# Kernel optimization log

Measured on AMD Instinct MI355X. Metric: run time of the kernel, lower is better.

## Reference

```python
import jax, jax.numpy as jnp
import numpy as np

MIN_RANGE, MAX_RANGE = -128.0, 127.0
B, S, F_IN, F_OUT = 4, 2048, 4096, 4096
ROUNDS, FACTOR = 12, 2  # 4096 = 2**12 -> 12 prime factors of 2
NBLK = F_IN // FACTOR   # 2048 blocks of 2x2 per round


def setup_inputs() -> dict:
    key = jax.random.key(0)
    ks = jax.random.split(key, 5)
    x = jax.random.normal(ks[0], (B, S, F_IN), jnp.float32)
    weight = jax.random.normal(ks[1], (F_OUT, F_IN), jnp.float32) * (1.0 / np.sqrt(F_IN))
    bias = jax.random.normal(ks[2], (F_OUT,), jnp.float32)
    perm_keys = jax.random.split(ks[3], ROUNDS)
    permutations = jnp.stack([jax.random.permutation(k, F_IN) for k in perm_keys])  # (ROUNDS, F_IN) int32
    # random 2x2 orthogonal blocks via batched QR (stand-in for ortho_group.rvs)
    a = jax.random.normal(ks[4], (ROUNDS, NBLK, FACTOR, FACTOR), jnp.float32)
    matrices, _ = jnp.linalg.qr(a)  # (ROUNDS, NBLK, FACTOR, FACTOR)
    return {"x": x, "weight": weight, "bias": bias,
            "matrices": matrices, "permutations": permutations}


def _rotate(v, permutations, matrices):
    # v: (..., F_IN). Each round: permute features, then block-diagonal orthogonal matmul.
    for r in range(ROUNDS):
        v = v[..., permutations[r]]
        lead = v.shape[:-1]
        vb = v.reshape(lead + (NBLK, FACTOR))
        vb = jnp.einsum('kij,...kj->...ki', matrices[r], vb)
        v = vb.reshape(lead + (F_IN,))
    return v


def _quant_dequant(t):
    # per-tensor asymmetric quantization to [MIN_RANGE, MAX_RANGE] then dequant
    lo = t.min()
    hi = t.max()
    scale = (hi - lo) / (MAX_RANGE - MIN_RANGE)
    q = jnp.clip(jnp.round((t - lo) / scale) + MIN_RANGE, MIN_RANGE, MAX_RANGE)
    return (q - MIN_RANGE) * scale + lo


def reference(x, weight, bias, matrices, permutations):
    # permuted_x = permute_op(x.mT).mT  <=>  rotate along the feature (last) dim
    x_rot = _rotate(x, permutations, matrices)          # (B, S, F_IN)
    # permuted_weight = permute_op(W.mT, inv_mT).mT; for orthogonal blocks inv.mT == M
    w_rot = _rotate(weight, permutations, matrices)     # (F_OUT, F_IN)
    xq = _quant_dequant(x_rot)
    wq = _quant_dequant(w_rot)
    return jnp.einsum('bsf,of->bso', xq, wq) + bias     # (B, S, F_OUT)
```

## Files before the change

kernel.cpp:

```cpp
#include <hip/hip_runtime.h>

#define F_DIM  4096
#define NROUNDS 12
#define GM     8192
#define GN     4096
#define GK     4096
#define BK     64
#define NIT    (GK / BK)

typedef short short8 __attribute__((ext_vector_type(8)));
typedef float f32x4  __attribute__((ext_vector_type(4)));
typedef unsigned short us8 __attribute__((ext_vector_type(8)));
typedef unsigned short ushortT;

typedef __attribute__((address_space(3))) void lds_void;
typedef const __attribute__((address_space(1))) void glob_void;

__device__ __forceinline__ unsigned ordf(float f) {
    unsigned u = __float_as_uint(f);
    return (u & 0x80000000u) ? ~u : (u | 0x80000000u);
}
__device__ __forceinline__ float unordf(unsigned u) {
    unsigned v = (u & 0x80000000u) ? (u & 0x7fffffffu) : ~u;
    return __uint_as_float(v);
}
__device__ __forceinline__ unsigned f2bf(float f) {
    unsigned u = __float_as_uint(f);
    return ((u + 0x7fffu + ((u >> 16) & 1u)) >> 16) & 0xffffu;
}

__global__ void init_mm_kernel(unsigned* mm) {
    if (threadIdx.x < 4) mm[threadIdx.x] = (threadIdx.x & 1) ? 0u : 0xFFFFFFFFu;
}

__global__ __launch_bounds__(256)
void rotate_store_kernel(const float* __restrict__ src,
                         const int*   __restrict__ perms,
                         const float* __restrict__ mats,
                         unsigned*    __restrict__ mm,
                         ushortT*     __restrict__ dst_hi,
                         ushortT*     __restrict__ dst_lo)
{
    __shared__ float4 buf[F_DIM];
    const int t = threadIdx.x;
    const size_t r0 = (size_t)blockIdx.x * 4;
    const int2*   pbase = (const int2*)perms;
    const float4* mbase = (const float4*)mats;

    const float2* s0 = (const float2*)(src + (r0 + 0) * F_DIM);
    const float2* s1 = (const float2*)(src + (r0 + 1) * F_DIM);
    const float2* s2 = (const float2*)(src + (r0 + 2) * F_DIM);
    const float2* s3 = (const float2*)(src + (r0 + 3) * F_DIM);
    #pragma unroll
    for (int q = 0; q < 8; ++q) {
        const int e = t + q * 256;
        float2 a = s0[e], b = s1[e], c = s2[e], d = s3[e];
        buf[e]        = make_float4(a.x, b.x, c.x, d.x);
        buf[e + 2048] = make_float4(a.y, b.y, c.y, d.y);
    }
    __syncthreads();

    int2 pA[8], pB[8];
    float4 mA[8], mB[8];
    #pragma unroll
    for (int q = 0; q < 8; ++q) { int k = t + q * 256; pA[q] = pbase[k]; mA[q] = mbase[k]; }

    #pragma unroll 1
    for (int r = 0; r < NROUNDS; r += 2) {
        float4 va[8], vb[8];
        #pragma unroll
        for (int q = 0; q < 8; ++q) {
            int fa = pA[q].x, fb = pA[q].y;
            va[q] = buf[(fa >> 1) + ((fa & 1) << 11)];
            vb[q] = buf[(fb >> 1) + ((fb & 1) << 11)];
        }
        {
            const int2*   pr = pbase + (size_t)(r + 1) * 2048;
            const float4* mr = mbase + (size_t)(r + 1) * 2048;
            #pragma unroll
            for (int q = 0; q < 8; ++q) { int k = t + q * 256; pB[q] = pr[k]; mB[q] = mr[k]; }
        }
        __syncthreads();
        #pragma unroll
        for (int q = 0; q < 8; ++q) {
            const int k = t + q * 256;
            float4 A = va[q], B = vb[q], M = mA[q];
            buf[k]        = make_float4(M.x*A.x + M.y*B.x, M.x*A.y + M.y*B.y,
                                        M.x*A.z + M.y*B.z, M.x*A.w + M.y*B.w);
            buf[k + 2048] = make_float4(M.z*A.x + M.w*B.x, M.z*A.y + M.w*B.y,
                                        M.z*A.z + M.w*B.z, M.z*A.w + M.w*B.w);
        }
        __syncthreads();

        #pragma unroll
        for (int q = 0; q < 8; ++q) {
            int fa = pB[q].x, fb = pB[q].y;
            va[q] = buf[(fa >> 1) + ((fa & 1) << 11)];
            vb[q] = buf[(fb >> 1) + ((fb & 1) << 11)];
        }
        if (r + 2 < NROUNDS) {
            const int2*   pr = pbase + (size_t)(r + 2) * 2048;
            const float4* mr = mbase + (size_t)(r + 2) * 2048;
            #pragma unroll
            for (int q = 0; q < 8; ++q) { int k = t + q * 256; pA[q] = pr[k]; mA[q] = mr[k]; }
        }
        __syncthreads();
        #pragma unroll
        for (int q = 0; q < 8; ++q) {
            const int k = t + q * 256;
            float4 A = va[q], B = vb[q], M = mB[q];
            buf[k]        = make_float4(M.x*A.x + M.y*B.x, M.x*A.y + M.y*B.y,
                                        M.x*A.z + M.y*B.z, M.x*A.w + M.y*B.w);
            buf[k + 2048] = make_float4(M.z*A.x + M.w*B.x, M.z*A.y + M.w*B.y,
                                        M.z*A.z + M.w*B.z, M.z*A.w + M.w*B.w);
        }
        __syncthreads();
    }

    float lmin = __FLT_MAX__, lmax = -__FLT_MAX__;
    #pragma unroll
    for (int q = 0; q < 8; ++q) {
        const int e = t + q * 256;
        float4 f0 = buf[e];
        float4 f1 = buf[e + 2048];
        lmin = fminf(lmin, fminf(fminf(f0.x, f0.y), fminf(f0.z, f0.w)));
        lmin = fminf(lmin, fminf(fminf(f1.x, f1.y), fminf(f1.z, f1.w)));
        lmax = fmaxf(lmax, fmaxf(fmaxf(f0.x, f0.y), fmaxf(f0.z, f0.w)));
        lmax = fmaxf(lmax, fmaxf(fmaxf(f1.x, f1.y), fmaxf(f1.z, f1.w)));
        const float vr[4][2] = {{f0.x, f1.x}, {f0.y, f1.y}, {f0.z, f1.z}, {f0.w, f1.w}};
        #pragma unroll
        for (int i = 0; i < 4; ++i) {
            unsigned u0 = __float_as_uint(vr[i][0]);
            unsigned u1 = __float_as_uint(vr[i][1]);
            ((unsigned*)(dst_hi + (r0 + i) * F_DIM))[e] = (u0 >> 16) | (u1 & 0xffff0000u);
            ((unsigned*)(dst_lo + (r0 + i) * F_DIM))[e] = (u0 & 0xffffu) | (u1 << 16);
        }
    }
    #pragma unroll
    for (int off = 32; off > 0; off >>= 1) {
        lmin = fminf(lmin, __shfl_down(lmin, off));
        lmax = fmaxf(lmax, __shfl_down(lmax, off));
    }
    if ((t & 63) == 0) {
        atomicMin(&mm[0], ordf(lmin));
        atomicMax(&mm[1], ordf(lmax));
    }
}

__global__ __launch_bounds__(256)
void quant_kernel(ushortT* __restrict__ hi, const ushortT* __restrict__ lo,
                  const unsigned* __restrict__ mm, unsigned nx_chunks)
{
    const unsigned i = blockIdx.x * 256 + threadIdx.x;
    const int sel = (i < nx_chunks) ? 0 : 2;
    const float lov = unordf(mm[sel]);
    const float hiv = unordf(mm[sel + 1]);
    const float scale = (hiv - lov) / 255.0f;
    us8 h = *(const us8*)(hi + (size_t)i * 8);
    us8 l = *(const us8*)(lo + (size_t)i * 8);
    us8 o;
    #pragma unroll
    for (int j = 0; j < 8; ++j) {
        float f = __uint_as_float(((unsigned)h[j] << 16) | (unsigned)l[j]);
        float q = rintf((f - lov) / scale);
        q = fminf(fmaxf(q, 0.0f), 255.0f);
        o[j] = (ushortT)f2bf(q * scale + lov);
    }
    *(us8*)(hi + (size_t)i * 8) = o;
}

__global__ __launch_bounds__(256)
void gemm_bias_kernel(const ushortT* __restrict__ A,
                      const ushortT* __restrict__ B,
                      const float*   __restrict__ bias,
                      float*         __restrict__ C)
{
    __shared__ alignas(16) ushortT As[128 * 8 * 8];
    __shared__ alignas(16) ushortT Bs[128 * 8 * 8];
    const int t = threadIdx.x;
    const int bid = blockIdx.x;
    const int mb = (bid >> 8) * 8 + (bid & 7);
    const int nb = (bid >> 3) & 31;
    const int lane = t & 63, wv = t >> 6;
    const int wm = (wv & 1) * 64, wn = (wv >> 1) * 64;
    const int rr = lane & 15, kc = lane >> 4;

    const int srow = t >> 3;
    const int cg   = (t & 7) ^ (srow & 7);
    const ushortT* pa = A + ((size_t)(mb * 128 + srow) * GK) + cg * 8;
    const ushortT* pb = B + ((size_t)(nb * 128 + srow) * GK) + cg * 8;

    f32x4 acc[4][4];
    const f32x4 zz = {0.f, 0.f, 0.f, 0.f};
    #pragma unroll
    for (int mi = 0; mi < 4; ++mi)
        #pragma unroll
        for (int ni = 0; ni < 4; ++ni)
            acc[mi][ni] = zz;

    auto stage = [&](int k0) {
        #pragma unroll
        for (int j = 0; j < 4; ++j) {
            __builtin_amdgcn_global_load_lds(
                (glob_void*)(pa + (size_t)j * 32 * GK + k0),
                (lds_void*)&As[(wv * 64 + 256 * j) * 8], 16, 0, 0);
            __builtin_amdgcn_global_load_lds(
                (glob_void*)(pb + (size_t)j * 32 * GK + k0),
                (lds_void*)&Bs[(wv * 64 + 256 * j) * 8], 16, 0, 0);
        }
    };

    stage(0);
    #pragma unroll 1
    for (int it = 0; it < NIT; ++it) {
        __syncthreads();

        short8 af[2][4], bfr[2][4];
        #pragma unroll
        for (int kk = 0; kk < 2; ++kk) {
            #pragma unroll
            for (int mi = 0; mi < 4; ++mi)
                af[kk][mi] = *(const short8*)
                    &As[((wm + mi * 16 + rr) * 8 + ((kk * 4 + kc) ^ (rr & 7))) * 8];
            #pragma unroll
            for (int ni = 0; ni < 4; ++ni)
                bfr[kk][ni] = *(const short8*)
                    &Bs[((wn + ni * 16 + rr) * 8 + ((kk * 4 + kc) ^ (rr & 7))) * 8];
        }
        __syncthreads();

        if (it + 1 < NIT) stage((it + 1) * BK);

        #pragma unroll
        for (int kk = 0; kk < 2; ++kk)
            #pragma unroll
            for (int mi = 0; mi < 4; ++mi)
                #pragma unroll
                for (int ni = 0; ni < 4; ++ni)
                    acc[mi][ni] = __builtin_amdgcn_mfma_f32_16x16x32_bf16(
                        af[kk][mi], bfr[kk][ni], acc[mi][ni], 0, 0, 0);
    }

    float bv[4];
    #pragma unroll
    for (int ni = 0; ni < 4; ++ni)
        bv[ni] = bias[nb * 128 + wn + ni * 16 + rr];

    #pragma unroll
    for (int mi = 0; mi < 4; ++mi) {
        #pragma unroll
        for (int ni = 0; ni < 4; ++ni) {
            const int col = nb * 128 + wn + ni * 16 + rr;
            #pragma unroll
            for (int r = 0; r < 4; ++r) {
                const int row = mb * 128 + wm + mi * 16 + kc * 4 + r;
                C[(size_t)row * GN + col] = acc[mi][ni][r] + bv[ni];
            }
        }
    }
}

extern "C" void kernel_launch(void* const* d_in, const int* in_sizes, int n_in,
                              void* d_out, int out_size, void* d_ws, size_t ws_size,
                              hipStream_t stream)
{
    (void)in_sizes; (void)n_in; (void)out_size; (void)ws_size;
    const float* x     = (const float*)d_in[0];
    const float* w     = (const float*)d_in[1];
    const float* bias  = (const float*)d_in[2];
    const float* mats  = (const float*)d_in[3];
    const int*   perms = (const int*)d_in[4];
    float* out = (float*)d_out;

    char* ws = (char*)d_ws;
    ushortT*  xq = (ushortT*)ws;
    ushortT*  wq = xq + (size_t)GM * GK;
    unsigned* mm = (unsigned*)(wq + (size_t)GN * GK);
    ushortT*  xlo = (ushortT*)out;
    ushortT*  wlo = xlo + (size_t)GM * GK;

    init_mm_kernel<<<1, 64, 0, stream>>>(mm);
    rotate_store_kernel<<<GM / 4, 256, 0, stream>>>(x, perms, mats, mm + 0, xq, xlo);
    rotate_store_kernel<<<GN / 4, 256, 0, stream>>>(w, perms, mats, mm + 2, wq, wlo);
    quant_kernel<<<(GM + GN) * (GK / 8) / 256, 256, 0, stream>>>(
        xq, xlo, mm, (unsigned)((size_t)GM * GK / 8));
    gemm_bias_kernel<<<GM / 128 * GN / 128, 256, 0, stream>>>(xq, wq, bias, out);
}
```

Before: 869.2 us.

## Replace bf16 dequantized GEMM with int8 MFMA GEMM plus affine correction

Quantized values are now stored as int8 codes, with per-row code sums, in place of dequantized bf16. The GEMM runs on i32 int8 MFMA (16x16x64) at double the K per tile, and the epilogue rebuilds the dequantized product from the scales, offsets, row sums and column sums. This halves operand bytes and uses the higher-throughput int8 MFMA path. The trade-off is an fp32 intermediate round-trip through memory and per-row quant kernels, and the result can drift slightly from the bf16-rounded path because the int accumulation is exact.

```diff
diff --git a/kernel.cpp b/kernel.cpp
--- a/kernel.cpp
+++ b/kernel.cpp
@@ -5,13 +5,11 @@
 #define GM     8192
 #define GN     4096
 #define GK     4096
-#define BK     64
-#define NIT    (GK / BK)
-
-typedef short short8 __attribute__((ext_vector_type(8)));
-typedef float f32x4  __attribute__((ext_vector_type(4)));
-typedef unsigned short us8 __attribute__((ext_vector_type(8)));
-typedef unsigned short ushortT;
+#define BK2    128
+#define NIT2   (GK / BK2)
+
+typedef int  int4v __attribute__((ext_vector_type(4)));
+typedef signed char schar;
 
 typedef __attribute__((address_space(3))) void lds_void;
 typedef const __attribute__((address_space(1))) void glob_void;
@@ -23,10 +21,6 @@
 __device__ __forceinline__ float unordf(unsigned u) {
     unsigned v = (u & 0x80000000u) ? (u & 0x7fffffffu) : ~u;
     return __uint_as_float(v);
-}
-__device__ __forceinline__ unsigned f2bf(float f) {
-    unsigned u = __float_as_uint(f);
-    return ((u + 0x7fffu + ((u >> 16) & 1u)) >> 16) & 0xffffu;
 }
 
 __global__ void init_mm_kernel(unsigned* mm) {
@@ -38,8 +32,7 @@
                          const int*   __restrict__ perms,
                          const float* __restrict__ mats,
                          unsigned*    __restrict__ mm,
-                         ushortT*     __restrict__ dst_hi,
-                         ushortT*     __restrict__ dst_lo)
+                         float*       __restrict__ dst)
 {
     __shared__ float4 buf[F_DIM];
     const int t = threadIdx.x;
@@ -127,14 +120,10 @@
         lmin = fminf(lmin, fminf(fminf(f1.x, f1.y), fminf(f1.z, f1.w)));
         lmax = fmaxf(lmax, fmaxf(fmaxf(f0.x, f0.y), fmaxf(f0.z, f0.w)));
         lmax = fmaxf(lmax, fmaxf(fmaxf(f1.x, f1.y), fmaxf(f1.z, f1.w)));
-        const float vr[4][2] = {{f0.x, f1.x}, {f0.y, f1.y}, {f0.z, f1.z}, {f0.w, f1.w}};
-        #pragma unroll
-        for (int i = 0; i < 4; ++i) {
-            unsigned u0 = __float_as_uint(vr[i][0]);
-            unsigned u1 = __float_as_uint(vr[i][1]);
-            ((unsigned*)(dst_hi + (r0 + i) * F_DIM))[e] = (u0 >> 16) | (u1 & 0xffff0000u);
-            ((unsigned*)(dst_lo + (r0 + i) * F_DIM))[e] = (u0 & 0xffffu) | (u1 << 16);
-        }
+        ((float2*)(dst + (r0 + 0) * F_DIM))[e] = make_float2(f0.x, f1.x);
+        ((float2*)(dst + (r0 + 1) * F_DIM))[e] = make_float2(f0.y, f1.y);
+        ((float2*)(dst + (r0 + 2) * F_DIM))[e] = make_float2(f0.z, f1.z);
+        ((float2*)(dst + (r0 + 3) * F_DIM))[e] = make_float2(f0.w, f1.w);
     }
     #pragma unroll
     for (int off = 32; off > 0; off >>= 1) {
@@ -148,35 +137,52 @@
 }
 
 __global__ __launch_bounds__(256)
-void quant_kernel(ushortT* __restrict__ hi, const ushortT* __restrict__ lo,
-                  const unsigned* __restrict__ mm, unsigned nx_chunks)
+void quant_row_kernel(const float* __restrict__ src,
+                      schar*       __restrict__ dst,
+                      int*         __restrict__ rowsum,
+                      const unsigned* __restrict__ mm, int sel)
 {
-    const unsigned i = blockIdx.x * 256 + threadIdx.x;
-    const int sel = (i < nx_chunks) ? 0 : 2;
-    const float lov = unordf(mm[sel]);
-    const float hiv = unordf(mm[sel + 1]);
-    const float scale = (hiv - lov) / 255.0f;
-    us8 h = *(const us8*)(hi + (size_t)i * 8);
-    us8 l = *(const us8*)(lo + (size_t)i * 8);
-    us8 o;
-    #pragma unroll
-    for (int j = 0; j < 8; ++j) {
-        float f = __uint_as_float(((unsigned)h[j] << 16) | (unsigned)l[j]);
-        float q = rintf((f - lov) / scale);
-        q = fminf(fmaxf(q, 0.0f), 255.0f);
-        o[j] = (ushortT)f2bf(q * scale + lov);
-    }
-    *(us8*)(hi + (size_t)i * 8) = o;
+    const int row = blockIdx.x, t = threadIdx.x;
+    const float lo = unordf(mm[sel]);
+    const float hi = unordf(mm[sel + 1]);
+    const float scale = (hi - lo) / 255.0f;
+    const float4* s = (const float4*)(src + (size_t)row * F_DIM);
+    unsigned* d = (unsigned*)(dst + (size_t)row * F_DIM);
+    int sum = 0;
+    #pragma unroll
+    for (int j = 0; j < 4; ++j) {
+        const int c = t + 256 * j;
+        float4 v = s[c];
+        int p0 = (int)fminf(fmaxf(rintf((v.x - lo) / scale), 0.0f), 255.0f);
+        int p1 = (int)fminf(fmaxf(rintf((v.y - lo) / scale), 0.0f), 255.0f);
+        int p2 = (int)fminf(fmaxf(rintf((v.z - lo) / scale), 0.0f), 255.0f);
+        int p3 = (int)fminf(fmaxf(rintf((v.w - lo) / scale), 0.0f), 255.0f);
+        sum += p0 + p1 + p2 + p3 - 512;
+        unsigned pack = ((unsigned)(p0 - 128) & 0xffu)
+                      | (((unsigned)(p1 - 128) & 0xffu) << 8)
+                      | (((unsigned)(p2 - 128) & 0xffu) << 16)
+                      | (((unsigned)(p3 - 128) & 0xffu) << 24);
+        d[c] = pack;
+    }
+    #pragma unroll
+    for (int off = 32; off > 0; off >>= 1) sum += __shfl_down(sum, off);
+    __shared__ int part[4];
+    if ((t & 63) == 0) part[t >> 6] = sum;
+    __syncthreads();
+    if (t == 0) rowsum[row] = part[0] + part[1] + part[2] + part[3];
 }
 
 __global__ __launch_bounds__(256)
-void gemm_bias_kernel(const ushortT* __restrict__ A,
-                      const ushortT* __restrict__ B,
-                      const float*   __restrict__ bias,
-                      float*         __restrict__ C)
+void gemm_i8_bias_kernel(const schar* __restrict__ A,
+                         const schar* __restrict__ B,
+                         const float* __restrict__ bias,
+                         const int*   __restrict__ Rx,
+                         const int*   __restrict__ Rw,
+                         const unsigned* __restrict__ mm,
+                         float*       __restrict__ C)
 {
-    __shared__ alignas(16) ushortT As[128 * 8 * 8];
-    __shared__ alignas(16) ushortT Bs[128 * 8 * 8];
+    __shared__ alignas(16) schar As[128 * 8 * 16];
+    __shared__ alignas(16) schar Bs[128 * 8 * 16];
     const int t = threadIdx.x;
     const int bid = blockIdx.x;
     const int mb = (bid >> 8) * 8 + (bid & 7);
@@ -187,11 +193,11 @@
 
     const int srow = t >> 3;
     const int cg   = (t & 7) ^ (srow & 7);
-    const ushortT* pa = A + ((size_t)(mb * 128 + srow) * GK) + cg * 8;
-    const ushortT* pb = B + ((size_t)(nb * 128 + srow) * GK) + cg * 8;
-
-    f32x4 acc[4][4];
-    const f32x4 zz = {0.f, 0.f, 0.f, 0.f};
+    const schar* pa = A + ((size_t)(mb * 128 + srow) * GK) + cg * 16;
+    const schar* pb = B + ((size_t)(nb * 128 + srow) * GK) + cg * 16;
+
+    int4v acc[4][4];
+    const int4v zz = {0, 0, 0, 0};
     #pragma unroll
     for (int mi = 0; mi < 4; ++mi)
         #pragma unroll
@@ -203,33 +209,33 @@
         for (int j = 0; j < 4; ++j) {
             __builtin_amdgcn_global_load_lds(
                 (glob_void*)(pa + (size_t)j * 32 * GK + k0),
-                (lds_void*)&As[(wv * 64 + 256 * j) * 8], 16, 0, 0);
+                (lds_void*)&As[(size_t)(wv * 64 + 256 * j) * 16], 16, 0, 0);
             __builtin_amdgcn_global_load_lds(
                 (glob_void*)(pb + (size_t)j * 32 * GK + k0),
-                (lds_void*)&Bs[(wv * 64 + 256 * j) * 8], 16, 0, 0);
+                (lds_void*)&Bs[(size_t)(wv * 64 + 256 * j) * 16], 16, 0, 0);
         }
     };
 
     stage(0);
     #pragma unroll 1
-    for (int it = 0; it < NIT; ++it) {
-        __syncthreads();
-
-        short8 af[2][4], bfr[2][4];
+    for (int it = 0; it < NIT2; ++it) {
+        __syncthreads();
+
+        int4v af[2][4], bfr[2][4];
         #pragma unroll
         for (int kk = 0; kk < 2; ++kk) {
             #pragma unroll
             for (int mi = 0; mi < 4; ++mi)
-                af[kk][mi] = *(const short8*)
-                    &As[((wm + mi * 16 + rr) * 8 + ((kk * 4 + kc) ^ (rr & 7))) * 8];
+                af[kk][mi] = *(const int4v*)
+                    &As[(size_t)((wm + mi * 16 + rr) * 8 + ((kk * 4 + kc) ^ (rr & 7))) * 16];
             #pragma unroll
             for (int ni = 0; ni < 4; ++ni)
-                bfr[kk][ni] = *(const short8*)
-                    &Bs[((wn + ni * 16 + rr) * 8 + ((kk * 4 + kc) ^ (rr & 7))) * 8];
-        }
-        __syncthreads();
-
-        if (it + 1 < NIT) stage((it + 1) * BK);
+                bfr[kk][ni] = *(const int4v*)
+                    &Bs[(size_t)((wn + ni * 16 + rr) * 8 + ((kk * 4 + kc) ^ (rr & 7))) * 16];
+        }
+        __syncthreads();
+
+        if (it + 1 < NIT2) stage((it + 1) * BK2);
 
         #pragma unroll
         for (int kk = 0; kk < 2; ++kk)
@@ -237,14 +243,30 @@
             for (int mi = 0; mi < 4; ++mi)
                 #pragma unroll
                 for (int ni = 0; ni < 4; ++ni)
-                    acc[mi][ni] = __builtin_amdgcn_mfma_f32_16x16x32_bf16(
+                    acc[mi][ni] = __builtin_amdgcn_mfma_i32_16x16x64_i8(
                         af[kk][mi], bfr[kk][ni], acc[mi][ni], 0, 0, 0);
     }
 
-    float bv[4];
-    #pragma unroll
-    for (int ni = 0; ni < 4; ++ni)
-        bv[ni] = bias[nb * 128 + wn + ni * 16 + rr];
+    const float lox = unordf(mm[0]), hix = unordf(mm[1]);
+    const float low = unordf(mm[2]), hiw = unordf(mm[3]);
+    const float ax = (hix - lox) / 255.0f, aw = (hiw - low) / 255.0f;
+    const float cx = 128.0f * ax + lox, cw = 128.0f * aw + low;
+    const float sxw = ax * aw;
+    const float kcc = (float)GK * cx * cw;
+    const float axcw = ax * cw, awcx = aw * cx;
+
+    float colt[4];
+    #pragma unroll
+    for (int ni = 0; ni < 4; ++ni) {
+        const int col = nb * 128 + wn + ni * 16 + rr;
+        colt[ni] = awcx * (float)Rw[col] + kcc + bias[col];
+    }
+    float rowt[4][4];
+    #pragma unroll
+    for (int mi = 0; mi < 4; ++mi)
+        #pragma unroll
+        for (int r = 0; r < 4; ++r)
+            rowt[mi][r] = axcw * (float)Rx[mb * 128 + wm + mi * 16 + kc * 4 + r];
 
     #pragma unroll
     for (int mi = 0; mi < 4; ++mi) {
@@ -254,7 +276,8 @@
             #pragma unroll
             for (int r = 0; r < 4; ++r) {
                 const int row = mb * 128 + wm + mi * 16 + kc * 4 + r;
-                C[(size_t)row * GN + col] = acc[mi][ni][r] + bv[ni];
+                C[(size_t)row * GN + col] =
+                    sxw * (float)acc[mi][ni][r] + rowt[mi][r] + colt[ni];
             }
         }
     }
@@ -273,16 +296,19 @@
     float* out = (float*)d_out;
 
     char* ws = (char*)d_ws;
-    ushortT*  xq = (ushortT*)ws;
-    ushortT*  wq = xq + (size_t)GM * GK;
-    unsigned* mm = (unsigned*)(wq + (size_t)GN * GK);
-    ushortT*  xlo = (ushortT*)out;
-    ushortT*  wlo = xlo + (size_t)GM * GK;
+    float*    wrot = (float*)ws;
+    schar*    xq8  = (schar*)ws;
+    int*      Rx   = (int*)(ws + (size_t)32 * 1024 * 1024);
+    schar*    wq8  = (schar*)(ws + (size_t)64 * 1024 * 1024);
+    int*      Rw   = (int*)(ws + (size_t)80 * 1024 * 1024);
+    unsigned* mm   = (unsigned*)(ws + (size_t)81 * 1024 * 1024);
+    float*    xrot = out;
 
     init_mm_kernel<<<1, 64, 0, stream>>>(mm);
-    rotate_store_kernel<<<GM / 4, 256, 0, stream>>>(x, perms, mats, mm + 0, xq, xlo);
-    rotate_store_kernel<<<GN / 4, 256, 0, stream>>>(w, perms, mats, mm + 2, wq, wlo);
-    quant_kernel<<<(GM + GN) * (GK / 8) / 256, 256, 0, stream>>>(
-        xq, xlo, mm, (unsigned)((size_t)GM * GK / 8));
-    gemm_bias_kernel<<<GM / 128 * GN / 128, 256, 0, stream>>>(xq, wq, bias, out);
-}
+    rotate_store_kernel<<<GN / 4, 256, 0, stream>>>(w, perms, mats, mm + 2, wrot);
+    quant_row_kernel<<<GN, 256, 0, stream>>>(wrot, wq8, Rw, mm, 2);
+    rotate_store_kernel<<<GM / 4, 256, 0, stream>>>(x, perms, mats, mm + 0, xrot);
+    quant_row_kernel<<<GM, 256, 0, stream>>>(xrot, xq8, Rx, mm, 0);
+    gemm_i8_bias_kernel<<<GM / 128 * GN / 128, 256, 0, stream>>>(
+        xq8, wq8, bias, Rx, Rw, mm, out);
+}
```

Result: faster. 718.7 us (-17.3%).
